# Optimization experiments

Measured on AMD Instinct MI355X. Metric: run time of the kernel, lower is better.

The kernel has to match this reference:

```python
import jax, jax.numpy as jnp
import numpy as np

# Hard-coded video-latent geometry from the module's tile/untile rearranges
NT, NH, NW = 6, 6, 6          # tile grid
TT, TH, TW = 6, 8, 8          # tile sizes (6*8*8 = 384 tokens per tile)
TILE = TT * TH * TW           # 384
NTILES = NT * NH * NW         # 216
SEQ = NTILES * TILE           # 82944 = 36*48*48
# per-head sliding-tile windows (w_t, w_h, w_w), i.e. mask_strategy (sp_size=1)
WINDOWS = ((2, 1, 1), (1, 2, 2), (1, 1, 2), (1, 1, 1))


def tile(x):
    # 'b (t h w) head d' with (t,h,w)=(36,48,48) ->
    # 'b (n_t n_h n_w ts_t ts_h ts_w) head d'  (sp_size = 1)
    b, s, H, d = x.shape
    x = x.reshape(b, NT, TT, NH, TH, NW, TW, H, d)
    x = x.transpose(0, 1, 3, 5, 2, 4, 6, 7, 8)  # b, nt, nh, nw, tst, tsh, tsw, H, d
    return x.reshape(b, s, H, d)


def untile(x):
    b, s, H, d = x.shape
    x = x.reshape(b, NT, NH, NW, TT, TH, TW, H, d)
    x = x.transpose(0, 1, 4, 2, 5, 3, 6, 7, 8)  # b, nt, tst, nh, tsh, nw, tsw, H, d
    return x.reshape(b, s, H, d)


def _axis_window(w, n):
    # allowed key tile indices per query tile along one axis, clamped at borders
    q = jnp.arange(n)
    start = jnp.clip(q - (w - 1) // 2, 0, n - w)
    return start[:, None] + jnp.arange(w)[None, :]  # [n, w]


def _tile_gather_idx(wt, wh, ww):
    # flat key-tile ids [NTILES, wt*wh*ww] for every query tile
    it = _axis_window(wt, NT)  # [NT, wt]
    ih = _axis_window(wh, NH)  # [NH, wh]
    iw = _axis_window(ww, NW)  # [NW, ww]
    idx = (it[:, None, None, :, None, None] * (NH * NW)
           + ih[None, :, None, None, :, None] * NW
           + iw[None, None, :, None, None, :])
    return idx.reshape(NTILES, wt * wh * ww)


def sliding_tile_attention(q, k, v):
    # q, k, v: [B, S, H, d] in TILED order; returns [B, S, H, d] tiled order
    B, S, H, d = q.shape
    scale = 1.0 / jnp.sqrt(jnp.asarray(d, q.dtype))
    qt = q.reshape(B, NTILES, TILE, H, d)
    kt = k.reshape(B, NTILES, TILE, H, d)
    vt = v.reshape(B, NTILES, TILE, H, d)
    outs = []
    for h, (wt, wh, ww) in enumerate(WINDOWS):
        idx = _tile_gather_idx(wt, wh, ww)            # [NTILES, W]
        qh = qt[:, :, :, h, :]                        # [B, Q, 384, d]
        kg = kt[:, :, :, h, :][:, idx]                # [B, Q, W, 384, d]
        vg = vt[:, :, :, h, :][:, idx]
        W = idx.shape[1]
        kg = kg.reshape(B, NTILES, W * TILE, d)
        vg = vg.reshape(B, NTILES, W * TILE, d)
        s = jnp.einsum('bqnd,bqmd->bqnm', qh, kg) * scale
        p = jax.nn.softmax(s, axis=-1)
        outs.append(jnp.einsum('bqnm,bqmd->bqnd', p, vg))
    o = jnp.stack(outs, axis=3)                       # [B, Q, 384, H, d]
    return o.reshape(B, S, H, d)


def setup_inputs() -> dict:
    key = jax.random.key(0)
    kq, kk, kv = jax.random.split(key, 3)
    B, H, d = 1, 4, 64
    q = jax.random.normal(kq, (B, SEQ, H, d), dtype=jnp.float32)
    k = jax.random.normal(kk, (B, SEQ, H, d), dtype=jnp.float32)
    v = jax.random.normal(kv, (B, SEQ, H, d), dtype=jnp.float32)
    return {'q': q, 'k': k, 'v': v}


def reference(q, k, v):
    # parallel_attn_func, STA branch, sp_size = 1 (no sequence parallelism)
    qt_, kt_, vt_ = tile(q), tile(k), tile(v)
    x = sliding_tile_attention(qt_, kt_, vt_)
    return untile(x)
```

## Files before the change

kernel.cpp:

```cpp
#include <hip/hip_runtime.h>

typedef _Float16 half4 __attribute__((ext_vector_type(4)));
typedef _Float16 half8 __attribute__((ext_vector_type(8)));
typedef float    f32x4 __attribute__((ext_vector_type(4)));
typedef unsigned int u32x2 __attribute__((ext_vector_type(2)));
typedef unsigned int u32x4 __attribute__((ext_vector_type(4)));

__device__ __forceinline__ unsigned int pkrtz(float a, float b) {
    return __builtin_bit_cast(unsigned int, __builtin_amdgcn_cvt_pkrtz(a, b));
}
__device__ __forceinline__ half4 pack4(float a, float b, float c, float d) {
    u32x2 t; t[0] = pkrtz(a, b); t[1] = pkrtz(c, d);
    return __builtin_bit_cast(half4, t);
}
__device__ __forceinline__ half8 cat8(half4 lo, half4 hi) {
    u32x2 l = __builtin_bit_cast(u32x2, lo), h = __builtin_bit_cast(u32x2, hi);
    u32x4 t; t[0] = l[0]; t[1] = l[1]; t[2] = h[0]; t[3] = h[1];
    return __builtin_bit_cast(half8, t);
}
__device__ __forceinline__ float fexp2(float x) {
    return __builtin_amdgcn_exp2f(x);
}

#define ROWF 256
#define HDIM 64

__device__ __forceinline__ int intra_off(int j) {
    return 2304 * (j >> 6) + 48 * ((j >> 3) & 7) + (j & 7);
}

__device__ __forceinline__ int kperm(int x) {
    return (x & 0x23) | ((x & 0x18) >> 1) | ((x & 4) << 2);
}

__global__ __launch_bounds__(512) void sta_kernel(
    const float* __restrict__ qg, const float* __restrict__ kg,
    const float* __restrict__ vg, float* __restrict__ out)
{
    __shared__ _Float16 Klds[128 * 64];
    __shared__ _Float16 Vlds[64 * 128];

    const int tid  = threadIdx.x;
    const int wave = tid >> 6;
    const int lane = tid & 63;
    const int g    = lane >> 4;
    const int c    = lane & 15;
    const int csw  = c >> 1;

    const int bid  = blockIdx.x;
    const int hidx = bid / 216;
    const int tile = bid - hidx * 216;
    const int head = (hidx == 0) ? 1 : (hidx == 1 ? 0 : hidx);

    const int nt = tile / 36;
    const int nh = (tile / 6) % 6;
    const int nw = tile % 6;
    const int tbase = 13824 * nt + 384 * nh + 8 * nw;

    int W, kb0; unsigned long long dpk;
    const int t0 = nt < 4 ? nt : 4;
    const int h0 = nh < 4 ? nh : 4;
    const int w0 = nw < 4 ? nw : 4;
    if (head == 0) {
        W = 2; kb0 = 13824 * t0 + 384 * nh + 8 * nw; dpk = (13824ULL << 16);
    } else if (head == 1) {
        W = 4; kb0 = 13824 * nt + 384 * h0 + 8 * w0;
        dpk = (8ULL << 16) | (384ULL << 32) | (392ULL << 48);
    } else if (head == 2) {
        W = 2; kb0 = 13824 * nt + 384 * nh + 8 * w0; dpk = (8ULL << 16);
    } else {
        W = 1; kb0 = tbase; dpk = 0ULL;
    }
    const int NC = W * 3;

    const float qscale = 0.125f * 1.44269504f;
    half8 qf[3][2];
    #pragma unroll
    for (int mt = 0; mt < 3; ++mt) {
        const int j = wave * 48 + mt * 16 + c;
        const float* qp = qg + (size_t)(tbase + intra_off(j)) * ROWF + head * HDIM;
        #pragma unroll
        for (int kc = 0; kc < 2; ++kc) {
            f32x4 a = *(const f32x4*)(qp + kc * 32 + g * 8);
            f32x4 b = *(const f32x4*)(qp + kc * 32 + g * 8 + 4);
            u32x4 t;
            t[0] = pkrtz(a[0] * qscale, a[1] * qscale);
            t[1] = pkrtz(a[2] * qscale, a[3] * qscale);
            t[2] = pkrtz(b[0] * qscale, b[1] * qscale);
            t[3] = pkrtz(b[2] * qscale, b[3] * qscale);
            qf[mt][kc] = __builtin_bit_cast(half8, t);
        }
    }

    u32x4 onep; onep[0] = onep[1] = onep[2] = onep[3] = 0x3C003C00u;
    const half8 ones8 = __builtin_bit_cast(half8, onep);

    f32x4 oacc[3][4];
    f32x4 lacc[3];
    float m_r[3];
    #pragma unroll
    for (int mt = 0; mt < 3; ++mt) {
        #pragma unroll
        for (int dt = 0; dt < 4; ++dt) oacc[mt][dt] = (f32x4){0.f, 0.f, 0.f, 0.f};
        lacc[mt] = (f32x4){0.f, 0.f, 0.f, 0.f};
        m_r[mt] = 8.0f;
    }

    const int r4  = tid >> 4;
    const int sc4 = tid & 15;

    int toff0, toff1, toff2, toff3, krow0;
    {
        const int r0 = r4 * 4;
        toff0 = intra_off(r0 + 0);
        toff1 = intra_off(r0 + 1);
        toff2 = intra_off(r0 + 2);
        toff3 = intra_off(r0 + 3);
        krow0 = (r0 & 64) + kperm(r0 & 63);
    }
    const size_t lin = (size_t)head * HDIM + sc4 * 4;

    f32x4 kr0, kr1, kr2, kr3, vr0, vr1, vr2, vr3;

#define ISSUE_N(N) do {                                                  \
        const int wi_ = (N) / 3;                                         \
        const int kb_ = kb0 + (int)((dpk >> (wi_ * 16)) & 0xFFFFULL)     \
                            + 4608 * ((N) - wi_ * 3);                    \
        const size_t a0 = (size_t)(kb_ + toff0) * ROWF + lin;            \
        const size_t a1 = (size_t)(kb_ + toff1) * ROWF + lin;            \
        const size_t a2 = (size_t)(kb_ + toff2) * ROWF + lin;            \
        const size_t a3 = (size_t)(kb_ + toff3) * ROWF + lin;            \
        kr0 = *(const f32x4*)(kg + a0); vr0 = *(const f32x4*)(vg + a0);  \
        kr1 = *(const f32x4*)(kg + a1); vr1 = *(const f32x4*)(vg + a1);  \
        kr2 = *(const f32x4*)(kg + a2); vr2 = *(const f32x4*)(vg + a2);  \
        kr3 = *(const f32x4*)(kg + a3); vr3 = *(const f32x4*)(vg + a3);  \
    } while (0)

#define COMMIT() do {                                                        \
        _Pragma("unroll")                                                    \
        for (int j = 0; j < 4; ++j) {                                        \
            const int kr_ = krow0 + j;                                       \
            const int ko_ = kr_ * 64 +                                       \
                (((sc4 >> 1) ^ ((kr_ >> 1) & 7)) << 3) + ((sc4 & 1) << 2);   \
            const f32x4 kv = (j == 0) ? kr0 : (j == 1) ? kr1                 \
                             : (j == 2) ? kr2 : kr3;                         \
            *(half4*)&Klds[ko_] = pack4(kv[0], kv[1], kv[2], kv[3]);         \
        }                                                                    \
        _Pragma("unroll")                                                    \
        for (int e = 0; e < 4; ++e) {                                        \
            const int vr_ = sc4 * 4 + e;                                     \
            const int vo_ = vr_ * 128 +                                      \
                (((r4 >> 1) ^ ((vr_ >> 1) & 7)) << 3) + ((r4 & 1) << 2);     \
            *(half4*)&Vlds[vo_] = pack4(vr0[e], vr1[e], vr2[e], vr3[e]);     \
        }                                                                    \
    } while (0)

    ISSUE_N(0);

    for (int ci = 0; ci < NC; ++ci) {
        COMMIT();
        __syncthreads();
        if (ci + 1 < NC) ISSUE_N(ci + 1);

        #pragma unroll
        for (int sub = 0; sub < 2; ++sub) {
            #pragma unroll
            for (int mt = 0; mt < 3; ++mt) {
                const float nm = -m_r[mt];
                f32x4 sacc[4];
                #pragma unroll
                for (int jt = 0; jt < 4; ++jt) sacc[jt] = (f32x4){nm, nm, nm, nm};
                #pragma unroll
                for (int kc = 0; kc < 2; ++kc) {
                    const half8 qfr = qf[mt][kc];
                    #pragma unroll
                    for (int jt = 0; jt < 4; ++jt) {
                        const half8 kf = *(const half8*)
                            &Klds[(sub * 64 + jt * 16 + c) * 64 + (((kc * 4 + g) ^ csw) << 3)];
                        sacc[jt] = __builtin_amdgcn_mfma_f32_16x16x32_f16(kf, qfr, sacc[jt], 0, 0, 0);
                    }
                }

                float p[4][4];
                #pragma unroll
                for (int jt = 0; jt < 4; ++jt)
                    #pragma unroll
                    for (int e = 0; e < 4; ++e)
                        p[jt][e] = fexp2(sacc[jt][e]);

                float m0 = fmaxf(fmaxf(fmaxf(sacc[0][0], sacc[0][1]), sacc[0][2]), sacc[0][3]);
                float m1 = fmaxf(fmaxf(fmaxf(sacc[1][0], sacc[1][1]), sacc[1][2]), sacc[1][3]);
                float m2 = fmaxf(fmaxf(fmaxf(sacc[2][0], sacc[2][1]), sacc[2][2]), sacc[2][3]);
                float m3 = fmaxf(fmaxf(fmaxf(sacc[3][0], sacc[3][1]), sacc[3][2]), sacc[3][3]);
                const float mm = fmaxf(fmaxf(fmaxf(m0, m1), m2), m3);

                if (__builtin_expect(!__all(mm <= 12.f), 0)) {
                    float mrow = mm;
                    mrow = fmaxf(mrow, __shfl_xor(mrow, 16, 64));
                    mrow = fmaxf(mrow, __shfl_xor(mrow, 32, 64));
                    const float delta = fmaxf(mrow, 0.f);
                    const float alpha = fexp2(-delta);
                    m_r[mt] += delta;
                    #pragma unroll
                    for (int jt = 0; jt < 4; ++jt)
                        #pragma unroll
                        for (int e = 0; e < 4; ++e)
                            p[jt][e] *= alpha;
                    float ar[4];
                    #pragma unroll
                    for (int r = 0; r < 4; ++r) ar[r] = __shfl(alpha, g * 4 + r, 16);
                    #pragma unroll
                    for (int r = 0; r < 4; ++r) {
                        lacc[mt][r] *= ar[r];
                        #pragma unroll
                        for (int dt = 0; dt < 4; ++dt)
                            oacc[mt][dt][r] *= ar[r];
                    }
                }

                half4 ph[4];
                #pragma unroll
                for (int jt = 0; jt < 4; ++jt)
                    ph[jt] = pack4(p[jt][0], p[jt][1], p[jt][2], p[jt][3]);

                #pragma unroll
                for (int kc = 0; kc < 2; ++kc) {
                    const half8 pa = cat8(ph[2 * kc], ph[2 * kc + 1]);
                    lacc[mt] = __builtin_amdgcn_mfma_f32_16x16x32_f16(pa, ones8, lacc[mt], 0, 0, 0);
                    #pragma unroll
                    for (int dt = 0; dt < 4; ++dt) {
                        const half8 vb = *(const half8*)
                            &Vlds[(dt * 16 + c) * 128 + (((sub * 8 + kc * 4 + g) ^ csw) << 3)];
                        oacc[mt][dt] = __builtin_amdgcn_mfma_f32_16x16x32_f16(pa, vb, oacc[mt][dt], 0, 0, 0);
                    }
                }
            }
        }
        __syncthreads();
    }
#undef ISSUE_N
#undef COMMIT

    #pragma unroll
    for (int mt = 0; mt < 3; ++mt) {
        #pragma unroll
        for (int r = 0; r < 4; ++r) {
            const int j = wave * 48 + mt * 16 + g * 4 + r;
            float* op = out + (size_t)(tbase + intra_off(j)) * ROWF + head * HDIM;
            const float linv = __builtin_amdgcn_rcpf(lacc[mt][r]);
            #pragma unroll
            for (int dt = 0; dt < 4; ++dt)
                op[dt * 16 + c] = oacc[mt][dt][r] * linv;
        }
    }
}

extern "C" void kernel_launch(void* const* d_in, const int* in_sizes, int n_in,
                              void* d_out, int out_size, void* d_ws, size_t ws_size,
                              hipStream_t stream) {
    const float* q = (const float*)d_in[0];
    const float* k = (const float*)d_in[1];
    const float* v = (const float*)d_in[2];
    float* o = (float*)d_out;
    dim3 grid(216 * 4);
    dim3 block(512);
    hipLaunchKernelGGL(sta_kernel, grid, block, 0, stream, q, k, v, o);
}
```

Before: 136.0 us.

## Restructure attention inner loop into 32-key steps with shared K/V fragments and VALU row sums

The inner loop now processes 32 keys per step instead of 64, and the K permutation is changed to match. Each K fragment loaded from LDS is reused across all three query tiles, and each V fragment across all three P operands, which cuts LDS reads. The row-sum MFMA against a ones vector is replaced by per-lane scalar accumulation with a cross-lane reduction at the end, removing a quarter of the PV-stage MFMAs. In exchange it adds VALU adds and shuffles, and keeps more accumulators live at once, which may raise register pressure.

```diff
diff --git a/kernel.cpp b/kernel.cpp
--- a/kernel.cpp
+++ b/kernel.cpp
@@ -13,9 +13,10 @@
     u32x2 t; t[0] = pkrtz(a, b); t[1] = pkrtz(c, d);
     return __builtin_bit_cast(half4, t);
 }
-__device__ __forceinline__ half8 cat8(half4 lo, half4 hi) {
-    u32x2 l = __builtin_bit_cast(u32x2, lo), h = __builtin_bit_cast(u32x2, hi);
-    u32x4 t; t[0] = l[0]; t[1] = l[1]; t[2] = h[0]; t[3] = h[1];
+__device__ __forceinline__ half8 pack8(float a, float b, float c, float d,
+                                       float e, float f, float gg, float h) {
+    u32x4 t; t[0] = pkrtz(a, b); t[1] = pkrtz(c, d);
+    t[2] = pkrtz(e, f); t[3] = pkrtz(gg, h);
     return __builtin_bit_cast(half8, t);
 }
 __device__ __forceinline__ float fexp2(float x) {
@@ -29,8 +30,8 @@
     return 2304 * (j >> 6) + 48 * ((j >> 3) & 7) + (j & 7);
 }
 
-__device__ __forceinline__ int kperm(int x) {
-    return (x & 0x23) | ((x & 0x18) >> 1) | ((x & 4) << 2);
+__device__ __forceinline__ int kperm32(int x) {
+    return ((x & 4) << 2) | ((x & 24) >> 1) | (x & 3);
 }
 
 __global__ __launch_bounds__(512) void sta_kernel(
@@ -83,27 +84,19 @@
         for (int kc = 0; kc < 2; ++kc) {
             f32x4 a = *(const f32x4*)(qp + kc * 32 + g * 8);
             f32x4 b = *(const f32x4*)(qp + kc * 32 + g * 8 + 4);
-            u32x4 t;
-            t[0] = pkrtz(a[0] * qscale, a[1] * qscale);
-            t[1] = pkrtz(a[2] * qscale, a[3] * qscale);
-            t[2] = pkrtz(b[0] * qscale, b[1] * qscale);
-            t[3] = pkrtz(b[2] * qscale, b[3] * qscale);
-            qf[mt][kc] = __builtin_bit_cast(half8, t);
+            qf[mt][kc] = pack8(a[0] * qscale, a[1] * qscale, a[2] * qscale, a[3] * qscale,
+                               b[0] * qscale, b[1] * qscale, b[2] * qscale, b[3] * qscale);
         }
     }
 
-    u32x4 onep; onep[0] = onep[1] = onep[2] = onep[3] = 0x3C003C00u;
-    const half8 ones8 = __builtin_bit_cast(half8, onep);
-
     f32x4 oacc[3][4];
-    f32x4 lacc[3];
-    float m_r[3];
+    float m_r[3], l_r[3];
     #pragma unroll
     for (int mt = 0; mt < 3; ++mt) {
         #pragma unroll
         for (int dt = 0; dt < 4; ++dt) oacc[mt][dt] = (f32x4){0.f, 0.f, 0.f, 0.f};
-        lacc[mt] = (f32x4){0.f, 0.f, 0.f, 0.f};
         m_r[mt] = 8.0f;
+        l_r[mt] = 0.f;
     }
 
     const int r4  = tid >> 4;
@@ -116,7 +109,7 @@
         toff1 = intra_off(r0 + 1);
         toff2 = intra_off(r0 + 2);
         toff3 = intra_off(r0 + 3);
-        krow0 = (r0 & 64) + kperm(r0 & 63);
+        krow0 = (r0 & 96) + kperm32(r0 & 31);
     }
     const size_t lin = (size_t)head * HDIM + sc4 * 4;
 
@@ -163,36 +156,39 @@
         if (ci + 1 < NC) ISSUE_N(ci + 1);
 
         #pragma unroll
-        for (int sub = 0; sub < 2; ++sub) {
+        for (int s = 0; s < 4; ++s) {
+            f32x4 sacc[3][2];
             #pragma unroll
             for (int mt = 0; mt < 3; ++mt) {
                 const float nm = -m_r[mt];
-                f32x4 sacc[4];
+                sacc[mt][0] = (f32x4){nm, nm, nm, nm};
+                sacc[mt][1] = (f32x4){nm, nm, nm, nm};
+            }
+            #pragma unroll
+            for (int kc = 0; kc < 2; ++kc) {
                 #pragma unroll
-                for (int jt = 0; jt < 4; ++jt) sacc[jt] = (f32x4){nm, nm, nm, nm};
-                #pragma unroll
-                for (int kc = 0; kc < 2; ++kc) {
-                    const half8 qfr = qf[mt][kc];
+                for (int jt = 0; jt < 2; ++jt) {
+                    const half8 kf = *(const half8*)
+                        &Klds[(s * 32 + jt * 16 + c) * 64 + (((kc * 4 + g) ^ csw) << 3)];
                     #pragma unroll
-                    for (int jt = 0; jt < 4; ++jt) {
-                        const half8 kf = *(const half8*)
-                            &Klds[(sub * 64 + jt * 16 + c) * 64 + (((kc * 4 + g) ^ csw) << 3)];
-                        sacc[jt] = __builtin_amdgcn_mfma_f32_16x16x32_f16(kf, qfr, sacc[jt], 0, 0, 0);
-                    }
+                    for (int mt = 0; mt < 3; ++mt)
+                        sacc[mt][jt] = __builtin_amdgcn_mfma_f32_16x16x32_f16(
+                            kf, qf[mt][kc], sacc[mt][jt], 0, 0, 0);
                 }
-
-                float p[4][4];
-                #pragma unroll
-                for (int jt = 0; jt < 4; ++jt)
-                    #pragma unroll
-                    for (int e = 0; e < 4; ++e)
-                        p[jt][e] = fexp2(sacc[jt][e]);
-
-                float m0 = fmaxf(fmaxf(fmaxf(sacc[0][0], sacc[0][1]), sacc[0][2]), sacc[0][3]);
-                float m1 = fmaxf(fmaxf(fmaxf(sacc[1][0], sacc[1][1]), sacc[1][2]), sacc[1][3]);
-                float m2 = fmaxf(fmaxf(fmaxf(sacc[2][0], sacc[2][1]), sacc[2][2]), sacc[2][3]);
-                float m3 = fmaxf(fmaxf(fmaxf(sacc[3][0], sacc[3][1]), sacc[3][2]), sacc[3][3]);
-                const float mm = fmaxf(fmaxf(fmaxf(m0, m1), m2), m3);
+            }
+
+            half8 pa[3];
+            #pragma unroll
+            for (int mt = 0; mt < 3; ++mt) {
+                float p0 = fexp2(sacc[mt][0][0]), p1 = fexp2(sacc[mt][0][1]);
+                float p2 = fexp2(sacc[mt][0][2]), p3 = fexp2(sacc[mt][0][3]);
+                float p4 = fexp2(sacc[mt][1][0]), p5 = fexp2(sacc[mt][1][1]);
+                float p6 = fexp2(sacc[mt][1][2]), p7 = fexp2(sacc[mt][1][3]);
+                const float ma = fmaxf(fmaxf(fmaxf(sacc[mt][0][0], sacc[mt][0][1]),
+                                             sacc[mt][0][2]), sacc[mt][0][3]);
+                const float mb = fmaxf(fmaxf(fmaxf(sacc[mt][1][0], sacc[mt][1][1]),
+                                             sacc[mt][1][2]), sacc[mt][1][3]);
+                const float mm = fmaxf(ma, mb);
 
                 if (__builtin_expect(!__all(mm <= 12.f), 0)) {
                     float mrow = mm;
@@ -201,39 +197,31 @@
                     const float delta = fmaxf(mrow, 0.f);
                     const float alpha = fexp2(-delta);
                     m_r[mt] += delta;
-                    #pragma unroll
-                    for (int jt = 0; jt < 4; ++jt)
-                        #pragma unroll
-                        for (int e = 0; e < 4; ++e)
-                            p[jt][e] *= alpha;
+                    l_r[mt] *= alpha;
+                    p0 *= alpha; p1 *= alpha; p2 *= alpha; p3 *= alpha;
+                    p4 *= alpha; p5 *= alpha; p6 *= alpha; p7 *= alpha;
                     float ar[4];
                     #pragma unroll
                     for (int r = 0; r < 4; ++r) ar[r] = __shfl(alpha, g * 4 + r, 16);
                     #pragma unroll
-                    for (int r = 0; r < 4; ++r) {
-                        lacc[mt][r] *= ar[r];
+                    for (int r = 0; r < 4; ++r)
                         #pragma unroll
                         for (int dt = 0; dt < 4; ++dt)
                             oacc[mt][dt][r] *= ar[r];
-                    }
                 }
 
-                half4 ph[4];
+                l_r[mt] += ((p0 + p1) + (p2 + p3)) + ((p4 + p5) + (p6 + p7));
+                pa[mt] = pack8(p0, p1, p2, p3, p4, p5, p6, p7);
+            }
+
+            #pragma unroll
+            for (int dt = 0; dt < 4; ++dt) {
+                const half8 vb = *(const half8*)
+                    &Vlds[(dt * 16 + c) * 128 + ((((s << 2) | g) ^ csw) << 3)];
                 #pragma unroll
-                for (int jt = 0; jt < 4; ++jt)
-                    ph[jt] = pack4(p[jt][0], p[jt][1], p[jt][2], p[jt][3]);
-
-                #pragma unroll
-                for (int kc = 0; kc < 2; ++kc) {
-                    const half8 pa = cat8(ph[2 * kc], ph[2 * kc + 1]);
-                    lacc[mt] = __builtin_amdgcn_mfma_f32_16x16x32_f16(pa, ones8, lacc[mt], 0, 0, 0);
-                    #pragma unroll
-                    for (int dt = 0; dt < 4; ++dt) {
-                        const half8 vb = *(const half8*)
-                            &Vlds[(dt * 16 + c) * 128 + (((sub * 8 + kc * 4 + g) ^ csw) << 3)];
-                        oacc[mt][dt] = __builtin_amdgcn_mfma_f32_16x16x32_f16(pa, vb, oacc[mt][dt], 0, 0, 0);
-                    }
-                }
+                for (int mt = 0; mt < 3; ++mt)
+                    oacc[mt][dt] = __builtin_amdgcn_mfma_f32_16x16x32_f16(
+                        pa[mt], vb, oacc[mt][dt], 0, 0, 0);
             }
         }
         __syncthreads();
@@ -243,11 +231,17 @@
 
     #pragma unroll
     for (int mt = 0; mt < 3; ++mt) {
+        float lf = l_r[mt];
+        lf += __shfl_xor(lf, 16, 64);
+        lf += __shfl_xor(lf, 32, 64);
+        float lq[4];
+        #pragma unroll
+        for (int r = 0; r < 4; ++r) lq[r] = __shfl(lf, g * 4 + r, 16);
         #pragma unroll
         for (int r = 0; r < 4; ++r) {
             const int j = wave * 48 + mt * 16 + g * 4 + r;
             float* op = out + (size_t)(tbase + intra_off(j)) * ROWF + head * HDIM;
-            const float linv = __builtin_amdgcn_rcpf(lacc[mt][r]);
+            const float linv = __builtin_amdgcn_rcpf(lq[r]);
             #pragma unroll
             for (int dt = 0; dt < 4; ++dt)
                 op[dt * 16 + c] = oacc[mt][dt][r] * linv;
```

Result: faster. 132.6 us (-2.5%).
